# Performance work log

Hardware: AMD Instinct MI355X
Metric: run time of the kernel (lower is better)

## Reference

```python
import jax, jax.numpy as jnp
import numpy as np
import math

B, S, E, H = 2, 2048, 1024, 16
D = E // H  # head_size = 64
EPS = 1e-5

def _ln(x, g, b):
    mu = jnp.mean(x, axis=-1, keepdims=True)
    var = jnp.mean(jnp.square(x - mu), axis=-1, keepdims=True)
    return (x - mu) * jax.lax.rsqrt(var + EPS) * g + b

def setup_inputs() -> dict:
    key = jax.random.key(0)
    ks = jax.random.split(key, 16)
    s = 0.02
    return {
        "I": jax.random.normal(ks[0], (B, S, E), jnp.float32),
        "x": jax.random.normal(ks[1], (B, S, E), jnp.float32),
        "mask": jnp.ones((B, 1, S), jnp.int32),
        # per-head Q/K/V weights stacked over heads [H, E, D], biases [H, D]
        "wq": jax.random.normal(ks[2], (H, E, D), jnp.float32) * s,
        "bq": jax.random.normal(ks[3], (H, D), jnp.float32) * s,
        "wk": jax.random.normal(ks[4], (H, E, D), jnp.float32) * s,
        "bk": jax.random.normal(ks[5], (H, D), jnp.float32) * s,
        "wv": jax.random.normal(ks[6], (H, E, D), jnp.float32) * s,
        "bv": jax.random.normal(ks[7], (H, D), jnp.float32) * s,
        "w_proj": jax.random.normal(ks[8], (E, E), jnp.float32) * s,
        "b_proj": jnp.zeros((E,), jnp.float32),
        "g1": jnp.ones((E,), jnp.float32),
        "be1": jnp.zeros((E,), jnp.float32),
        "g2": jnp.ones((E,), jnp.float32),
        "be2": jnp.zeros((E,), jnp.float32),
        "w1": jax.random.normal(ks[9], (E, 4 * E), jnp.float32) * s,
        "b1": jnp.zeros((4 * E,), jnp.float32),
        "w2": jax.random.normal(ks[10], (4 * E, E), jnp.float32) * s,
        "b2": jnp.zeros((E,), jnp.float32),
    }

def reference(I, x, mask, wq, bq, wk, bk, wv, bv, w_proj, b_proj,
              g1, be1, g2, be2, w1, b1, w2, b2):
    xn = _ln(x, g1, be1)
    # batched per-head projections: [B,S,E] x [H,E,D] -> [B,H,S,D]
    q = jnp.einsum('bse,hed->bhsd', I, wq) + bq[None, :, None, :]
    k = jnp.einsum('bse,hed->bhsd', xn, wk) + bk[None, :, None, :]
    v = jnp.einsum('bse,hed->bhsd', xn, wv) + bv[None, :, None, :]
    # NOTE: original scales by sqrt(n_embed), not sqrt(head_size)
    scores = jnp.einsum('bhqd,bhkd->bhqk', q, k) / math.sqrt(E)
    scores = jnp.where(mask[:, None, :, :] == 0, -1e9, scores)
    attn = jax.nn.softmax(scores, axis=-1)
    ctx = jnp.einsum('bhqk,bhkd->bhqd', attn, v)
    # concat heads: [B,S,H,D] -> [B,S,E]
    ctx = ctx.transpose(0, 2, 1, 3).reshape(B, S, E)
    attn_out = ctx @ w_proj + b_proj
    h = xn + attn_out
    h2 = _ln(h, g2, be2)
    ff = jax.nn.gelu(h2 @ w1 + b1, approximate=False) @ w2 + b2
    return h2 + ff
```

## Files before the change

### kernel.cpp

```cpp
#include <hip/hip_runtime.h>
#include <hip/hip_bf16.h>
#include <math.h>

typedef short short8 __attribute__((ext_vector_type(8)));
typedef short short4_t __attribute__((ext_vector_type(4)));
typedef float f32x4 __attribute__((ext_vector_type(4)));
typedef unsigned short u16;
typedef unsigned int u32;

#define B_ 2
#define S_ 2048
#define E_ 1024
#define H_ 16
#define D_ 64
#define TOK (B_*S_)

__device__ __forceinline__ float bf2f(u16 u) {
    union { unsigned int u; float f; } v; v.u = ((unsigned int)u) << 16; return v.f;
}
__device__ __forceinline__ u16 f2bf(float f) {
    union { float f; unsigned int u; } v; v.f = f;
    unsigned int r = v.u + 0x7fffu + ((v.u >> 16) & 1u);
    return (u16)(r >> 16);
}
__device__ __forceinline__ u32 fbits(float f) {
    union { float f; u32 u; } v; v.f = f; return v.u;
}
__device__ __forceinline__ void gl_lds16(const u16* g, short* l) {
    __builtin_amdgcn_global_load_lds(
        (const __attribute__((address_space(1))) unsigned int*)(g),
        (__attribute__((address_space(3))) unsigned int*)(l), 16, 0, 0);
}

__global__ __launch_bounds__(256) void convf_k(const float* __restrict__ s, u16* __restrict__ d)
{
    size_t i = ((size_t)blockIdx.x * 256 + threadIdx.x) * 8;
    f32x4 a = *(const f32x4*)(s + i);
    f32x4 b = *(const f32x4*)(s + i + 4);
    short8 r;
#pragma unroll
    for (int j = 0; j < 4; j++) { r[j] = (short)f2bf(a[j]); r[4 + j] = (short)f2bf(b[j]); }
    *(short8*)(d + i) = r;
}

__global__ __launch_bounds__(256) void tconv_k(
    const float* __restrict__ src, u16* __restrict__ dst,
    int K, int N, size_t zsrc, size_t zdst)
{
    __shared__ u16 t[64][72];
    src += (size_t)blockIdx.z * zsrc;
    dst += (size_t)blockIdx.z * zdst;
    int k0 = blockIdx.y * 64, n0 = blockIdx.x * 64;
    int tid = threadIdx.x;
    int kr = tid >> 4, nc = (tid & 15) * 4;
#pragma unroll
    for (int i = 0; i < 4; i++) {
        f32x4 v = *(const f32x4*)(src + (size_t)(k0 + kr + i * 16) * N + n0 + nc);
#pragma unroll
        for (int j = 0; j < 4; j++) t[kr + i * 16][nc + j] = f2bf(v[j]);
    }
    __syncthreads();
    int nr = tid >> 2, kg = (tid & 3) * 16;
    short8 r0, r1;
#pragma unroll
    for (int j = 0; j < 8; j++) { r0[j] = (short)t[kg + j][nr]; r1[j] = (short)t[kg + 8 + j][nr]; }
    u16* dp = dst + (size_t)(n0 + nr) * K + k0 + kg;
    *(short8*)(dp) = r0;
    *(short8*)(dp + 8) = r1;
}

__global__ __launch_bounds__(256) void tconvqkv_k(
    const float* __restrict__ wq, const float* __restrict__ wk,
    const float* __restrict__ wv, u16* __restrict__ dst)
{
    __shared__ u16 t[64][72];
    int z = blockIdx.z;
    int w = z >> 4, hh = z & 15;
    const float* src = (w == 0 ? wq : (w == 1 ? wk : wv)) + (size_t)hh * E_ * D_;
    u16* d = dst + (size_t)w * E_ * E_ + (size_t)hh * D_ * E_;
    int k0 = blockIdx.y * 64;
    int tid = threadIdx.x;
    int kr = tid >> 4, nc = (tid & 15) * 4;
#pragma unroll
    for (int i = 0; i < 4; i++) {
        f32x4 v = *(const f32x4*)(src + (size_t)(k0 + kr + i * 16) * D_ + nc);
#pragma unroll
        for (int j = 0; j < 4; j++) t[kr + i * 16][nc + j] = f2bf(v[j]);
    }
    __syncthreads();
    int nr = tid >> 2, kg = (tid & 3) * 16;
    short8 r0, r1;
#pragma unroll
    for (int j = 0; j < 8; j++) { r0[j] = (short)t[kg + j][nr]; r1[j] = (short)t[kg + 8 + j][nr]; }
    u16* dp = d + (size_t)nr * E_ + k0 + kg;
    *(short8*)(dp) = r0;
    *(short8*)(dp + 8) = r1;
}

__global__ __launch_bounds__(256) void vtrans_k(const u16* __restrict__ V, u16* __restrict__ Vt)
{
    __shared__ u16 t[64][72];
    int s0 = blockIdx.x * 64, h = blockIdx.y, b = blockIdx.z;
    int tid = threadIdx.x;
    int sr = tid >> 2, dc = (tid & 3) * 16;
    const u16* src = V + (size_t)b * S_ * E_ + (size_t)(s0 + sr) * E_ + h * D_ + dc;
    short8 v0 = *(const short8*)(src);
    short8 v1 = *(const short8*)(src + 8);
#pragma unroll
    for (int j = 0; j < 8; j++) { t[sr][dc + j] = v0[j]; t[sr][dc + 8 + j] = v1[j]; }
    __syncthreads();
    int dr = tid >> 2, sc = (tid & 3) * 16;
    short8 r0, r1;
#pragma unroll
    for (int j = 0; j < 8; j++) { r0[j] = (short)t[sc + j][dr]; r1[j] = (short)t[sc + 8 + j][dr]; }
    u16* dp = Vt + ((size_t)(b * H_ + h) * D_ + dr) * S_ + s0 + sc;
    *(short8*)(dp) = r0;
    *(short8*)(dp + 8) = r1;
}

__global__ __launch_bounds__(256) void maskprep_k(
    const int* __restrict__ mask, float* __restrict__ fb, int* __restrict__ ok)
{
    __shared__ unsigned char fl[256];
    int b = blockIdx.x;
    int tid = threadIdx.x;
    int base = tid * 8;
    unsigned all = 1;
#pragma unroll
    for (int j = 0; j < 8; j++) {
        int m = mask[b * S_ + base + j];
        fb[b * S_ + base + j] = m ? 0.f : -1e9f;
        all &= (m != 0) ? 1u : 0u;
    }
    fl[tid] = (unsigned char)all;
    __syncthreads();
    if (tid < 32) {
        unsigned a = 1;
#pragma unroll
        for (int j = 0; j < 8; j++) a &= fl[tid * 8 + j];
        ok[b * 32 + tid] = (int)a;
    }
}

template<int INF32>
__global__ __launch_bounds__(256) void ln_kernel(
    const void* __restrict__ xv, const float* __restrict__ g,
    const float* __restrict__ be, u16* __restrict__ y)
{
    int lane = threadIdx.x & 63, wave = threadIdx.x >> 6;
    int row = blockIdx.x * 4 + wave;
    int c0 = lane * 16;
    float v[16];
    if (INF32) {
        const float* xr = (const float*)xv + (size_t)row * E_ + c0;
#pragma unroll
        for (int i = 0; i < 4; i++) {
            f32x4 xx = *(const f32x4*)(xr + i * 4);
#pragma unroll
            for (int j = 0; j < 4; j++) v[i * 4 + j] = xx[j];
        }
    } else {
        const u16* xr = (const u16*)xv + (size_t)row * E_ + c0;
        short8 a = *(const short8*)(xr);
        short8 b = *(const short8*)(xr + 8);
#pragma unroll
        for (int j = 0; j < 8; j++) { v[j] = bf2f((u16)a[j]); v[8 + j] = bf2f((u16)b[j]); }
    }
    float s = 0.f, q = 0.f;
#pragma unroll
    for (int i = 0; i < 16; i++) { s += v[i]; q += v[i] * v[i]; }
#pragma unroll
    for (int off = 1; off < 64; off <<= 1) {
        s += __shfl_xor(s, off, 64);
        q += __shfl_xor(q, off, 64);
    }
    float mu = s * (1.0f / E_);
    float var = q * (1.0f / E_) - mu * mu;
    float rstd = rsqrtf(var + 1e-5f);
    u16* yr = y + (size_t)row * E_ + c0;
    short8 o0, o1;
#pragma unroll
    for (int j = 0; j < 8; j++) {
        o0[j] = (short)f2bf((v[j] - mu) * rstd * g[c0 + j] + be[c0 + j]);
        o1[j] = (short)f2bf((v[8 + j] - mu) * rstd * g[c0 + 8 + j] + be[c0 + 8 + j]);
    }
    *(short8*)(yr) = o0;
    *(short8*)(yr + 8) = o1;
}

template<int QKV, int GELU, int RX>
__global__ __launch_bounds__(512) void gemm8p_k(
    const u16* __restrict__ A, const u16* __restrict__ Axn,
    const u16* __restrict__ WT,
    const float* __restrict__ bq, const float* __restrict__ bk, const float* __restrict__ bv,
    u16* __restrict__ C, int M, int N, int K)
{
    __shared__ __align__(16) short As[2][256 * 64];
    __shared__ __align__(16) short Bs[2][256 * 64];
    int tid = threadIdx.x;
    int wave = tid >> 6, lane = tid & 63, quad = lane >> 4, l16 = lane & 15;
    int wm = wave >> 2, wn = wave & 3;

    int gx = gridDim.x, gy = gridDim.y;
    int lin = blockIdx.y * gx + blockIdx.x;
    int xcd = lin & 7, w = lin >> 3;
    int rw = gx / RX, rh = gy / (8 / RX);
    int bx = (xcd % RX) * rw + (w % rw);
    int by = (xcd / RX) * rh + (w / rw);
    int n0 = bx * 256, m0 = by * 256;

    int which = QKV ? (n0 >> 10) : 0;
    const u16* Ause = (QKV && which) ? Axn : A;
    const float* bias = QKV ? (which == 0 ? bq : (which == 1 ? bk : bv)) : bq;

    f32x4 acc[8][4];
#pragma unroll
    for (int m = 0; m < 8; m++)
#pragma unroll
        for (int n = 0; n < 4; n++)
            acc[m][n] = (f32x4){0.f, 0.f, 0.f, 0.f};

    int srow = lane >> 3, slot = lane & 7;
    const u16* Ag = Ause + (size_t)(m0 + wave * 16 + srow) * K + ((slot ^ srow) << 3);
    const u16* Bg = WT + (size_t)(n0 + wave * 16 + srow) * K + ((slot ^ srow) << 3);
    const size_t r8K = (size_t)8 * K, r128K = (size_t)128 * K, r136K = (size_t)136 * K;
    int wv = wave * 1024;
    int r7 = l16 & 7;
    int soff0 = (quad ^ r7) << 3;
    int soff1 = ((4 + quad) ^ r7) << 3;
    int arow = (wm * 128 + l16) * 64;
    int brow = (wn * 64 + l16) * 64;
    int NT = K >> 6;

#define GLA2P(P, BUF, H) do { \
    gl_lds16((P) + ((H) ? r128K : (size_t)0), &As[BUF][wv + (H) * 8192]); \
    gl_lds16((P) + ((H) ? r136K : r8K), &As[BUF][wv + (H) * 8192 + 512]); } while (0)
#define GLB2P(P, BUF, H) do { \
    gl_lds16((P) + ((H) ? r128K : (size_t)0), &Bs[BUF][wv + (H) * 8192]); \
    gl_lds16((P) + ((H) ? r136K : r8K), &Bs[BUF][wv + (H) * 8192 + 512]); } while (0)

#define PHASE(BUF, mb, GLSTMT, TAILSTMT) do { \
    __builtin_amdgcn_sched_barrier(0); \
    short8 af[2][2]; \
    af[0][0] = *(const short8*)(&As[BUF][arow + (mb) * 1024 + soff0]); \
    af[0][1] = *(const short8*)(&As[BUF][arow + (mb) * 1024 + soff1]); \
    af[1][0] = *(const short8*)(&As[BUF][arow + ((mb) + 1) * 1024 + soff0]); \
    af[1][1] = *(const short8*)(&As[BUF][arow + ((mb) + 1) * 1024 + soff1]); \
    GLSTMT; \
    __builtin_amdgcn_s_barrier(); \
    asm volatile("s_waitcnt lgkmcnt(0)" ::: "memory"); \
    __builtin_amdgcn_sched_barrier(0); \
    __builtin_amdgcn_s_setprio(1); \
    _Pragma("unroll") \
    for (int i_ = 0; i_ < 2; i_++) \
    _Pragma("unroll") \
    for (int n_ = 0; n_ < 4; n_++) { \
        acc[(mb) + i_][n_] = __builtin_amdgcn_mfma_f32_16x16x32_bf16(af[i_][0], bf[n_][0], acc[(mb) + i_][n_], 0, 0, 0); \
        acc[(mb) + i_][n_] = __builtin_amdgcn_mfma_f32_16x16x32_bf16(af[i_][1], bf[n_][1], acc[(mb) + i_][n_], 0, 0, 0); \
    } \
    __builtin_amdgcn_s_setprio(0); \
    __builtin_amdgcn_sched_barrier(0); \
    TAILSTMT; \
    __builtin_amdgcn_s_barrier(); \
} while (0)

#define KTILE(BUF, OBUF, TT, PAx, PBx) do { \
    short8 bf[4][2]; \
    __builtin_amdgcn_sched_barrier(0); \
    _Pragma("unroll") \
    for (int n = 0; n < 4; n++) { \
        bf[n][0] = *(const short8*)(&Bs[BUF][brow + n * 1024 + soff0]); \
        bf[n][1] = *(const short8*)(&Bs[BUF][brow + n * 1024 + soff1]); \
    } \
    PHASE(BUF, 0, \
        { if ((TT) + 1 < NT) GLA2P((PAx), OBUF, 0); asm volatile("s_waitcnt lgkmcnt(8)" ::: "memory"); }, {}); \
    PHASE(BUF, 2, { if ((TT) + 1 < NT) GLA2P((PAx), OBUF, 1); }, {}); \
    PHASE(BUF, 4, { if ((TT) + 2 < NT) GLB2P((PBx), BUF, 0); }, {}); \
    PHASE(BUF, 6, { if ((TT) + 2 < NT) GLB2P((PBx), BUF, 1); }, \
        { if ((TT) + 2 < NT) asm volatile("s_waitcnt vmcnt(4)" ::: "memory"); \
          else               asm volatile("s_waitcnt vmcnt(0)" ::: "memory"); }); \
} while (0)

    GLB2P(Bg, 0, 0); GLB2P(Bg, 0, 1);
    GLA2P(Ag, 0, 0); GLA2P(Ag, 0, 1);
    if (NT > 1) {
        GLB2P(Bg + 64, 1, 0); GLB2P(Bg + 64, 1, 1);
        asm volatile("s_waitcnt vmcnt(4)" ::: "memory");
    } else {
        asm volatile("s_waitcnt vmcnt(0)" ::: "memory");
    }
    __builtin_amdgcn_s_barrier();

    const u16* PA = Ag + 64;
    const u16* PB = Bg + 128;
    for (int t = 0; t < NT; t += 2) {
        KTILE(0, 1, t, PA, PB);
        KTILE(1, 0, t + 1, PA + 64, PB + 64);
        PA += 128; PB += 128;
    }

    u16* Cw = QKV ? (C + (size_t)which * (size_t)M * 1024) : C;
    int ostride = QKV ? 1024 : N;
#pragma unroll
    for (int m = 0; m < 8; m++) {
#pragma unroll
        for (int n = 0; n < 4; n++) {
            int colg = n0 + wn * 64 + n * 16 + l16;
            int col = QKV ? (colg & 1023) : colg;
            float bb = bias[col];
#pragma unroll
            for (int r = 0; r < 4; r++) {
                int row = m0 + wm * 128 + m * 16 + quad * 4 + r;
                float v = acc[m][n][r] + bb;
                if (QKV && which == 0) v *= 0.03125f;
                if (GELU) v = 0.5f * v * (1.0f + erff(v * 0.70710678118f));
                Cw[(size_t)row * ostride + col] = f2bf(v);
            }
        }
    }
#undef GLA2P
#undef GLB2P
#undef PHASE
#undef KTILE
}

__global__ __launch_bounds__(256) void gemmsk_k(
    const u16* __restrict__ A, const u16* __restrict__ WT,
    u16* __restrict__ P, int M, int N, int K, int Ks)
{
    __shared__ __align__(16) short a_sh[2][128 * 32];
    __shared__ __align__(16) short b_sh[2][128 * 32];
    int tid = threadIdx.x;
    int wave = tid >> 6, lane = tid & 63, quad = lane >> 4, l16 = lane & 15;
    int wm = wave >> 1, wn = wave & 1;
    int gx = gridDim.x;
    int lin = blockIdx.y * gx + blockIdx.x;
    int xcd = lin & 7, w = lin >> 3;
    int rh = gridDim.y >> 3;
    int bx = w % gx, by = xcd * rh + (w / gx);
    int m0 = by * 128, n0 = bx * 128;
    int koff = blockIdx.z * Ks;

    f32x4 acc[4][4];
#pragma unroll
    for (int mt = 0; mt < 4; mt++)
#pragma unroll
        for (int nt = 0; nt < 4; nt++)
            acc[mt][nt] = (f32x4){0.f, 0.f, 0.f, 0.f};

    int srow = lane >> 2;
    int c = ((lane & 3) ^ ((lane >> 3) & 3)) * 8;
    const u16* Ab = A + (size_t)(m0 + wave * 32 + srow) * K + koff + c;
    const u16* Bb = WT + (size_t)(n0 + wave * 32 + srow) * K + koff + c;
    short* al0 = &a_sh[0][wave * 1024];
    short* al1 = &a_sh[1][wave * 1024];
    short* bl0 = &b_sh[0][wave * 1024];
    short* bl1 = &b_sh[1][wave * 1024];
    int xo = (quad ^ ((l16 >> 1) & 3)) * 8;

    for (int kk = 0; kk < Ks; kk += 64) {
        __syncthreads();
        gl_lds16(Ab + kk, al0);
        gl_lds16(Ab + kk + (size_t)16 * K, al0 + 512);
        gl_lds16(Ab + kk + 32, al1);
        gl_lds16(Ab + kk + (size_t)16 * K + 32, al1 + 512);
        gl_lds16(Bb + kk, bl0);
        gl_lds16(Bb + kk + (size_t)16 * K, bl0 + 512);
        gl_lds16(Bb + kk + 32, bl1);
        gl_lds16(Bb + kk + (size_t)16 * K + 32, bl1 + 512);
        __syncthreads();

#pragma unroll
        for (int h = 0; h < 2; h++) {
            short8 af[4], bf8[4];
#pragma unroll
            for (int mt = 0; mt < 4; mt++)
                af[mt] = *(const short8*)(&a_sh[h][(wm * 64 + mt * 16 + l16) * 32 + xo]);
#pragma unroll
            for (int nt = 0; nt < 4; nt++)
                bf8[nt] = *(const short8*)(&b_sh[h][(wn * 64 + nt * 16 + l16) * 32 + xo]);
#pragma unroll
            for (int mt = 0; mt < 4; mt++)
#pragma unroll
                for (int nt = 0; nt < 4; nt++)
                    acc[mt][nt] = __builtin_amdgcn_mfma_f32_16x16x32_bf16(af[mt], bf8[nt], acc[mt][nt], 0, 0, 0);
        }
    }

    u16* Pz = P + (size_t)blockIdx.z * (size_t)M * N;
#pragma unroll
    for (int mt = 0; mt < 4; mt++) {
#pragma unroll
        for (int nt = 0; nt < 4; nt++) {
            int col = n0 + wn * 64 + nt * 16 + l16;
#pragma unroll
            for (int r = 0; r < 4; r++) {
                int row = m0 + wm * 64 + mt * 16 + quad * 4 + r;
                Pz[(size_t)row * N + col] = f2bf(acc[mt][nt][r]);
            }
        }
    }
}

__global__ __launch_bounds__(256) void combine2_k(
    const u16* __restrict__ P, const float* __restrict__ bias,
    const u16* __restrict__ res, float* __restrict__ out)
{
    const size_t MN = (size_t)TOK * E_;
    size_t i = ((size_t)blockIdx.x * 256 + threadIdx.x) * 8;
    int col = (int)(i & (E_ - 1));
    float v[8];
    f32x4 b0 = *(const f32x4*)(bias + col);
    f32x4 b1 = *(const f32x4*)(bias + col + 4);
    short8 rr = *(const short8*)(res + i);
#pragma unroll
    for (int j = 0; j < 4; j++) { v[j] = b0[j] + bf2f((u16)rr[j]); v[4 + j] = b1[j] + bf2f((u16)rr[4 + j]); }
#pragma unroll
    for (int z = 0; z < 2; z++) {
        short8 p = *(const short8*)(P + z * MN + i);
#pragma unroll
        for (int j = 0; j < 8; j++) v[j] += bf2f((u16)p[j]);
    }
    f32x4 o0, o1;
#pragma unroll
    for (int j = 0; j < 4; j++) { o0[j] = v[j]; o1[j] = v[4 + j]; }
    *(f32x4*)(out + i) = o0;
    *(f32x4*)(out + i + 4) = o1;
}

template<int GELU, int RES, int CF32>
__global__ __launch_bounds__(256) void gemm3_k(
    const u16* __restrict__ A, const u16* __restrict__ WT,
    const float* __restrict__ bias, const u16* __restrict__ res,
    void* __restrict__ Cv, int M, int N, int K)
{
    __shared__ __align__(16) short a_sh[2][128 * 32];
    __shared__ __align__(16) short b_sh[2][64 * 32];
    int tid = threadIdx.x;
    int wave = tid >> 6, lane = tid & 63, quad = lane >> 4, l16 = lane & 15;
    int wm = wave >> 1, wn = wave & 1;
    int m0 = blockIdx.y * 128, n0 = blockIdx.x * 64;

    f32x4 acc[4][2];
#pragma unroll
    for (int mt = 0; mt < 4; mt++)
#pragma unroll
        for (int nt = 0; nt < 2; nt++)
            acc[mt][nt] = (f32x4){0.f, 0.f, 0.f, 0.f};

    int srow = lane >> 2;
    int c = ((lane & 3) ^ ((lane >> 3) & 3)) * 8;
    const u16* Ab = A + (size_t)(m0 + wave * 32 + srow) * K + c;
    const u16* Bb = WT + (size_t)(n0 + wave * 16 + srow) * K + c;
    short* al0 = &a_sh[0][wave * 1024];
    short* al1 = &a_sh[1][wave * 1024];
    short* bl0 = &b_sh[0][wave * 512];
    short* bl1 = &b_sh[1][wave * 512];
    int xo = (quad ^ ((l16 >> 1) & 3)) * 8;

    for (int kk = 0; kk < K; kk += 64) {
        __syncthreads();
        gl_lds16(Ab + kk, al0);
        gl_lds16(Ab + kk + (size_t)16 * K, al0 + 512);
        gl_lds16(Ab + kk + 32, al1);
        gl_lds16(Ab + kk + (size_t)16 * K + 32, al1 + 512);
        gl_lds16(Bb + kk, bl0);
        gl_lds16(Bb + kk + 32, bl1);
        __syncthreads();

#pragma unroll
        for (int h = 0; h < 2; h++) {
            short8 af[4], bf8[2];
#pragma unroll
            for (int mt = 0; mt < 4; mt++)
                af[mt] = *(const short8*)(&a_sh[h][(wm * 64 + mt * 16 + l16) * 32 + xo]);
#pragma unroll
            for (int nt = 0; nt < 2; nt++)
                bf8[nt] = *(const short8*)(&b_sh[h][(wn * 32 + nt * 16 + l16) * 32 + xo]);
#pragma unroll
            for (int mt = 0; mt < 4; mt++)
#pragma unroll
                for (int nt = 0; nt < 2; nt++)
                    acc[mt][nt] = __builtin_amdgcn_mfma_f32_16x16x32_bf16(af[mt], bf8[nt], acc[mt][nt], 0, 0, 0);
        }
    }

#pragma unroll
    for (int mt = 0; mt < 4; mt++) {
#pragma unroll
        for (int nt = 0; nt < 2; nt++) {
            int col = n0 + wn * 32 + nt * 16 + l16;
            float bb = bias[col];
#pragma unroll
            for (int r = 0; r < 4; r++) {
                int row = m0 + wm * 64 + mt * 16 + quad * 4 + r;
                float v = acc[mt][nt][r] + bb;
                if (RES) v += bf2f(res[(size_t)row * N + col]);
                if (GELU) v = 0.5f * v * (1.0f + erff(v * 0.70710678118f));
                if (CF32) ((float*)Cv)[(size_t)row * N + col] = v;
                else ((u16*)Cv)[(size_t)row * N + col] = f2bf(v);
            }
        }
    }
}

__global__ __launch_bounds__(512) void attn_k(
    const u16* __restrict__ Q, const u16* __restrict__ K,
    const u16* __restrict__ Vt, const float* __restrict__ fb,
    const int* __restrict__ ok, u16* __restrict__ O)
{
    __shared__ __align__(16) short k_sh[2][2][64 * 32];
    __shared__ __align__(16) short v_sh[2][2][64 * 32];
    __shared__ __align__(16) short p_sh[8][16 * 72];
    int tid = threadIdx.x;
    int wave = tid >> 6, lane = tid & 63, quad = lane >> 4, l16 = lane & 15;
    int qb = blockIdx.x, h = blockIdx.y, b = blockIdx.z;
    int q0 = qb * 128;
    const u16* Qp = Q + (size_t)b * S_ * E_ + (size_t)h * D_;
    const u16* Kp = K + (size_t)b * S_ * E_ + (size_t)h * D_;
    const u16* Vtp = Vt + (size_t)(b * H_ + h) * D_ * S_;

    int qrow = q0 + wave * 16 + l16;
    short8 qf0 = *(const short8*)(Qp + (size_t)qrow * E_ + quad * 8);
    short8 qf1 = *(const short8*)(Qp + (size_t)qrow * E_ + 32 + quad * 8);

    f32x4 o[4];
#pragma unroll
    for (int dt = 0; dt < 4; dt++) o[dt] = (f32x4){0.f, 0.f, 0.f, 0.f};
    float rs_tot = 0.f;

    int sub = wave & 1, rblk = wave >> 1;
    int srow = lane >> 2;
    int c = ((lane & 3) ^ ((lane >> 3) & 3)) * 8;
    const u16* Kg = Kp + (size_t)(rblk * 16 + srow) * E_ + sub * 32 + c;
    const u16* Vg = Vtp + (size_t)(rblk * 16 + srow) * S_ + sub * 32 + c;
    short* kl0 = &k_sh[0][sub][rblk * 512];
    short* kl1 = &k_sh[1][sub][rblk * 512];
    short* vl0 = &v_sh[0][sub][rblk * 512];
    short* vl1 = &v_sh[1][sub][rblk * 512];

    gl_lds16(Kg, kl0);
    gl_lds16(Vg, vl0);
    __syncthreads();

    const float* fbb = fb + b * S_;
    const int* okb = ok + b * 32;
    int xo = (quad ^ ((l16 >> 1) & 3)) * 8;

    for (int kt = 0; kt < S_ / 64; kt++) {
        int cur = kt & 1;
        if (kt < 31) {
            gl_lds16(Kg + (size_t)(kt + 1) * 64 * E_, cur ? kl0 : kl1);
            gl_lds16(Vg + (kt + 1) * 64, cur ? vl0 : vl1);
        }

        f32x4 s[4];
#pragma unroll
        for (int mt = 0; mt < 4; mt++) {
            int ro = (mt * 16 + l16) * 32 + xo;
            short8 kf0 = *(const short8*)(&k_sh[cur][0][ro]);
            short8 kf1 = *(const short8*)(&k_sh[cur][1][ro]);
            s[mt] = __builtin_amdgcn_mfma_f32_16x16x32_bf16(kf0, qf0, (f32x4){0.f,0.f,0.f,0.f}, 0, 0, 0);
            s[mt] = __builtin_amdgcn_mfma_f32_16x16x32_bf16(kf1, qf1, s[mt], 0, 0, 0);
        }

        if (!okb[kt]) {
#pragma unroll
            for (int mt = 0; mt < 4; mt++)
#pragma unroll
                for (int r = 0; r < 4; r++)
                    s[mt][r] += fbb[kt * 64 + mt * 16 + quad * 4 + r];
        }

#pragma unroll
        for (int mt = 0; mt < 4; mt++) {
            float p0 = __expf(s[mt][0]);
            float p1 = __expf(s[mt][1]);
            float p2 = __expf(s[mt][2]);
            float p3 = __expf(s[mt][3]);
            rs_tot += (p0 + p1) + (p2 + p3);
            u32 u0 = __builtin_amdgcn_perm(fbits(p1), fbits(p0), 0x07060302u);
            u32 u1 = __builtin_amdgcn_perm(fbits(p3), fbits(p2), 0x07060302u);
            uint2 pk; pk.x = u0; pk.y = u1;
            *(uint2*)(&p_sh[wave][l16 * 72 + mt * 16 + quad * 4]) = pk;
        }

#pragma unroll
        for (int sk = 0; sk < 2; sk++) {
            short8 pf = *(const short8*)(&p_sh[wave][l16 * 72 + sk * 32 + quad * 8]);
#pragma unroll
            for (int dt = 0; dt < 4; dt++) {
                short8 vf = *(const short8*)(&v_sh[cur][sk][(dt * 16 + l16) * 32 + xo]);
                o[dt] = __builtin_amdgcn_mfma_f32_16x16x32_bf16(vf, pf, o[dt], 0, 0, 0);
            }
        }
        __syncthreads();
    }

    rs_tot += __shfl_xor(rs_tot, 16, 64);
    rs_tot += __shfl_xor(rs_tot, 32, 64);
    float inv = 1.0f / rs_tot;
    u16* Op = O + (size_t)b * S_ * E_ + (size_t)(q0 + wave * 16 + l16) * E_ + h * D_;
#pragma unroll
    for (int dt = 0; dt < 4; dt++) {
        short4_t pk;
#pragma unroll
        for (int r = 0; r < 4; r++) pk[r] = (short)f2bf(o[dt][r] * inv);
        *(short4_t*)(Op + dt * 16 + quad * 4) = pk;
    }
}

extern "C" void kernel_launch(void* const* d_in, const int* in_sizes, int n_in,
                              void* d_out, int out_size, void* d_ws, size_t ws_size,
                              hipStream_t stream)
{
    (void)in_sizes; (void)n_in; (void)out_size; (void)ws_size;
    const float* I      = (const float*)d_in[0];
    const float* x      = (const float*)d_in[1];
    const int*   mask   = (const int*)d_in[2];
    const float* wq     = (const float*)d_in[3];
    const float* bq     = (const float*)d_in[4];
    const float* wk     = (const float*)d_in[5];
    const float* bk     = (const float*)d_in[6];
    const float* wv     = (const float*)d_in[7];
    const float* bv     = (const float*)d_in[8];
    const float* w_proj = (const float*)d_in[9];
    const float* b_proj = (const float*)d_in[10];
    const float* g1     = (const float*)d_in[11];
    const float* be1    = (const float*)d_in[12];
    const float* g2     = (const float*)d_in[13];
    const float* be2    = (const float*)d_in[14];
    const float* w1     = (const float*)d_in[15];
    const float* b1     = (const float*)d_in[16];
    const float* w2     = (const float*)d_in[17];
    const float* b2     = (const float*)d_in[18];
    float* out = (float*)d_out;

    char* ws = (char*)d_ws;
    const size_t SZ = (size_t)TOK * E_;
    u16* xn   = (u16*)(ws);
    u16* qb_  = (u16*)(ws + SZ * 2);
    u16* kb_  = (u16*)(ws + SZ * 4);
    u16* vb_  = (u16*)(ws + SZ * 6);
    u16* Vt   = (u16*)(ws + SZ * 8);
    u16* Ibf  = (u16*)(ws + SZ * 8);
    u16* ctx  = (u16*)(ws + SZ * 6);
    u16* hb   = (u16*)(ws + SZ * 4);
    u16* h2   = (u16*)(ws);
    u16* a1   = (u16*)(ws + SZ * 2);
    u16* WTqkv  = (u16*)(ws + 40u * 1024 * 1024);
    u16* WTproj = (u16*)(ws + 46u * 1024 * 1024);
    u16* WT1    = (u16*)(ws + 48u * 1024 * 1024);
    u16* WT2    = (u16*)(ws + 56u * 1024 * 1024);
    u16* Pp     = (u16*)(ws + 40u * 1024 * 1024);
    float* fbm  = (float*)(ws + 40u * 1024 * 1024);
    int*   okm  = (int*)(ws + 40u * 1024 * 1024 + 16384);

    convf_k<<<dim3(TOK * E_ / (256 * 8)), 256, 0, stream>>>(I, Ibf);
    tconvqkv_k<<<dim3(1, 16, 48), 256, 0, stream>>>(wq, wk, wv, WTqkv);
    tconv_k<<<dim3(16, 16, 1), 256, 0, stream>>>(w_proj, WTproj, E_, E_, 0, 0);
    tconv_k<<<dim3(64, 16, 1), 256, 0, stream>>>(w1, WT1, E_, 4 * E_, 0, 0);
    tconv_k<<<dim3(16, 64, 1), 256, 0, stream>>>(w2, WT2, 4 * E_, E_, 0, 0);

    ln_kernel<1><<<TOK / 4, 256, 0, stream>>>(x, g1, be1, xn);

    gemm8p_k<1,0,2><<<dim3(12, TOK / 256), 512, 0, stream>>>(
        Ibf, xn, WTqkv, bq, bk, bv, qb_, TOK, 3072, E_);

    maskprep_k<<<dim3(B_), 256, 0, stream>>>(mask, fbm, okm);
    vtrans_k<<<dim3(S_ / 64, H_, B_), 256, 0, stream>>>(vb_, Vt);

    attn_k<<<dim3(S_ / 128, H_, B_), 512, 0, stream>>>(qb_, kb_, Vt, fbm, okm, ctx);

    gemm3_k<0,1,0><<<dim3(16, TOK / 128), 256, 0, stream>>>(
        ctx, WTproj, b_proj, xn, hb, TOK, E_, E_);
    ln_kernel<0><<<TOK / 4, 256, 0, stream>>>(hb, g2, be2, h2);
    gemm8p_k<0,1,2><<<dim3(16, TOK / 256), 512, 0, stream>>>(
        h2, nullptr, WT1, b1, nullptr, nullptr, a1, TOK, 4 * E_, E_);
    gemmsk_k<<<dim3(8, TOK / 128, 2), 256, 0, stream>>>(
        a1, WT2, Pp, TOK, E_, 4 * E_, 2 * E_);
    combine2_k<<<dim3(TOK * E_ / (256 * 8)), 256, 0, stream>>>(Pp, b2, h2, out);
}
```

Before: 376.8 us.

## Software-pipeline LDS fragment reads across MFMA phases in GEMM main loop

Restructures the GEMM k-tile loop so each phase's A-fragment LDS reads for the next phase are issued right after the current phase's MFMAs. This replaces a read-then-wait-then-compute pattern with overlapped reads. It halves the block barriers per k-tile from two per phase to one, drops the explicit lgkmcnt waits and leaves LDS wait insertion to the compiler. MFMA order is reordered so the k-halves alternate across two M rows, which eases register dependencies. Removing barriers and manual waits risks subtler buffer-reuse hazards and relies on compiler-inserted waitcnts.

Result: no change. 373.0 us (-1.0%).

```diff
diff --git a/kernel.cpp b/kernel.cpp
--- a/kernel.cpp
+++ b/kernel.cpp
@@ -232,53 +232,61 @@
     int brow = (wn * 64 + l16) * 64;
     int NT = K >> 6;
 
+#define SB __builtin_amdgcn_sched_barrier(0)
 #define GLA2P(P, BUF, H) do { \
     gl_lds16((P) + ((H) ? r128K : (size_t)0), &As[BUF][wv + (H) * 8192]); \
     gl_lds16((P) + ((H) ? r136K : r8K), &As[BUF][wv + (H) * 8192 + 512]); } while (0)
 #define GLB2P(P, BUF, H) do { \
     gl_lds16((P) + ((H) ? r128K : (size_t)0), &Bs[BUF][wv + (H) * 8192]); \
     gl_lds16((P) + ((H) ? r136K : r8K), &Bs[BUF][wv + (H) * 8192 + 512]); } while (0)
-
-#define PHASE(BUF, mb, GLSTMT, TAILSTMT) do { \
-    __builtin_amdgcn_sched_barrier(0); \
-    short8 af[2][2]; \
-    af[0][0] = *(const short8*)(&As[BUF][arow + (mb) * 1024 + soff0]); \
-    af[0][1] = *(const short8*)(&As[BUF][arow + (mb) * 1024 + soff1]); \
-    af[1][0] = *(const short8*)(&As[BUF][arow + ((mb) + 1) * 1024 + soff0]); \
-    af[1][1] = *(const short8*)(&As[BUF][arow + ((mb) + 1) * 1024 + soff1]); \
-    GLSTMT; \
-    __builtin_amdgcn_s_barrier(); \
-    asm volatile("s_waitcnt lgkmcnt(0)" ::: "memory"); \
-    __builtin_amdgcn_sched_barrier(0); \
-    __builtin_amdgcn_s_setprio(1); \
-    _Pragma("unroll") \
-    for (int i_ = 0; i_ < 2; i_++) \
+#define RDA(BUF, Mi, SO) (*(const short8*)(&As[BUF][arow + (Mi) * 1024 + (SO)]))
+#define RDB(BUF, Ni, SO) (*(const short8*)(&Bs[BUF][brow + (Ni) * 1024 + (SO)]))
+#define MM2(mb, R) do { \
     _Pragma("unroll") \
     for (int n_ = 0; n_ < 4; n_++) { \
-        acc[(mb) + i_][n_] = __builtin_amdgcn_mfma_f32_16x16x32_bf16(af[i_][0], bf[n_][0], acc[(mb) + i_][n_], 0, 0, 0); \
-        acc[(mb) + i_][n_] = __builtin_amdgcn_mfma_f32_16x16x32_bf16(af[i_][1], bf[n_][1], acc[(mb) + i_][n_], 0, 0, 0); \
+        acc[(mb)][n_]     = __builtin_amdgcn_mfma_f32_16x16x32_bf16(R[0], bf[n_][0], acc[(mb)][n_], 0, 0, 0); \
+        acc[(mb) + 1][n_] = __builtin_amdgcn_mfma_f32_16x16x32_bf16(R[1], bf[n_][0], acc[(mb) + 1][n_], 0, 0, 0); \
     } \
-    __builtin_amdgcn_s_setprio(0); \
-    __builtin_amdgcn_sched_barrier(0); \
-    TAILSTMT; \
-    __builtin_amdgcn_s_barrier(); \
+    _Pragma("unroll") \
+    for (int n_ = 0; n_ < 4; n_++) { \
+        acc[(mb)][n_]     = __builtin_amdgcn_mfma_f32_16x16x32_bf16(R[2], bf[n_][1], acc[(mb)][n_], 0, 0, 0); \
+        acc[(mb) + 1][n_] = __builtin_amdgcn_mfma_f32_16x16x32_bf16(R[3], bf[n_][1], acc[(mb) + 1][n_], 0, 0, 0); \
+    } \
 } while (0)
 
-#define KTILE(BUF, OBUF, TT, PAx, PBx) do { \
-    short8 bf[4][2]; \
-    __builtin_amdgcn_sched_barrier(0); \
-    _Pragma("unroll") \
-    for (int n = 0; n < 4; n++) { \
-        bf[n][0] = *(const short8*)(&Bs[BUF][brow + n * 1024 + soff0]); \
-        bf[n][1] = *(const short8*)(&Bs[BUF][brow + n * 1024 + soff1]); \
-    } \
-    PHASE(BUF, 0, \
-        { if ((TT) + 1 < NT) GLA2P((PAx), OBUF, 0); asm volatile("s_waitcnt lgkmcnt(8)" ::: "memory"); }, {}); \
-    PHASE(BUF, 2, { if ((TT) + 1 < NT) GLA2P((PAx), OBUF, 1); }, {}); \
-    PHASE(BUF, 4, { if ((TT) + 2 < NT) GLB2P((PBx), BUF, 0); }, {}); \
-    PHASE(BUF, 6, { if ((TT) + 2 < NT) GLB2P((PBx), BUF, 1); }, \
-        { if ((TT) + 2 < NT) asm volatile("s_waitcnt vmcnt(4)" ::: "memory"); \
-          else               asm volatile("s_waitcnt vmcnt(0)" ::: "memory"); }); \
+#define KTILE(BUF, OBUF, TT, AO, BO) do { \
+    SB; __builtin_amdgcn_s_barrier(); \
+    short8 bf[4][2], af[4], ag[4]; \
+     \
+    bf[0][0] = RDB(BUF, 0, soff0); bf[1][0] = RDB(BUF, 1, soff0); \
+    bf[2][0] = RDB(BUF, 2, soff0); bf[3][0] = RDB(BUF, 3, soff0); \
+    af[0] = RDA(BUF, 0, soff0); af[1] = RDA(BUF, 1, soff0); \
+    bf[0][1] = RDB(BUF, 0, soff1); bf[1][1] = RDB(BUF, 1, soff1); \
+    bf[2][1] = RDB(BUF, 2, soff1); bf[3][1] = RDB(BUF, 3, soff1); \
+    af[2] = RDA(BUF, 0, soff1); af[3] = RDA(BUF, 1, soff1); \
+    if ((TT) + 1 < NT) GLA2P((AO), OBUF, 0); \
+    __builtin_amdgcn_s_setprio(1); MM2(0, af); __builtin_amdgcn_s_setprio(0); \
+    ag[0] = RDA(BUF, 2, soff0); ag[1] = RDA(BUF, 3, soff0); \
+    ag[2] = RDA(BUF, 2, soff1); ag[3] = RDA(BUF, 3, soff1); \
+    SB; __builtin_amdgcn_s_barrier(); \
+     \
+    if ((TT) + 1 < NT) GLA2P((AO), OBUF, 1); \
+    __builtin_amdgcn_s_setprio(1); MM2(2, ag); __builtin_amdgcn_s_setprio(0); \
+    af[0] = RDA(BUF, 4, soff0); af[1] = RDA(BUF, 5, soff0); \
+    af[2] = RDA(BUF, 4, soff1); af[3] = RDA(BUF, 5, soff1); \
+    SB; __builtin_amdgcn_s_barrier(); \
+     \
+    if ((TT) + 2 < NT) GLB2P((BO), BUF, 0); \
+    __builtin_amdgcn_s_setprio(1); MM2(4, af); __builtin_amdgcn_s_setprio(0); \
+    ag[0] = RDA(BUF, 6, soff0); ag[1] = RDA(BUF, 7, soff0); \
+    ag[2] = RDA(BUF, 6, soff1); ag[3] = RDA(BUF, 7, soff1); \
+    SB; __builtin_amdgcn_s_barrier(); \
+     \
+    if ((TT) + 2 < NT) GLB2P((BO), BUF, 1); \
+    __builtin_amdgcn_s_setprio(1); MM2(6, ag); __builtin_amdgcn_s_setprio(0); \
+    if ((TT) + 2 < NT) { asm volatile("s_waitcnt vmcnt(4)" ::: "memory"); } \
+    else               { asm volatile("s_waitcnt vmcnt(0)" ::: "memory"); } \
+    SB; \
 } while (0)
 
     GLB2P(Bg, 0, 0); GLB2P(Bg, 0, 1);
@@ -289,14 +297,13 @@
     } else {
         asm volatile("s_waitcnt vmcnt(0)" ::: "memory");
     }
-    __builtin_amdgcn_s_barrier();
-
-    const u16* PA = Ag + 64;
-    const u16* PB = Bg + 128;
+
+    const u16* A1 = Ag + 64;
+    const u16* B2 = Bg + 128;
     for (int t = 0; t < NT; t += 2) {
-        KTILE(0, 1, t, PA, PB);
-        KTILE(1, 0, t + 1, PA + 64, PB + 64);
-        PA += 128; PB += 128;
+        KTILE(0, 1, t, A1, B2);
+        KTILE(1, 0, t + 1, A1 + 64, B2 + 64);
+        A1 += 128; B2 += 128;
     }
 
     u16* Cw = QKV ? (C + (size_t)which * (size_t)M * 1024) : C;
@@ -318,9 +325,12 @@
             }
         }
     }
+#undef SB
 #undef GLA2P
 #undef GLB2P
-#undef PHASE
+#undef RDA
+#undef RDB
+#undef MM2
 #undef KTILE
 }
 
```
